# Kernel tuning notes

Measured on AMD Instinct MI355X. Metric: run time of the kernel, lower is better.

## Reference

```python
import jax, jax.numpy as jnp
import numpy as np

N, E = 50000, 800000
F_IN, C1, H1 = 128, 16, 4        # conv1: 128 -> 16 per head, 4 heads (concat -> 64)
F_MID = C1 * H1                   # 64
N_CLASSES, H2 = 10, 1             # conv2: 64 -> 10, 1 head, no concat
NEG_SLOPE = 0.2


def setup_inputs() -> dict:
    key = jax.random.key(0)
    ks = jax.random.split(key, 12)
    s1 = 1.0 / np.sqrt(F_IN)
    s2 = 1.0 / np.sqrt(F_MID)
    return {
        "x": jax.random.normal(ks[0], (N, F_IN), dtype=jnp.float32),
        "edge_index": jax.random.randint(ks[1], (2, E), 0, N, dtype=jnp.int64),
        # conv1 params (GATv2: separate lin_l / lin_r, per-head attention vector, bias)
        "W1l": jax.random.normal(ks[2], (F_IN, H1 * C1), dtype=jnp.float32) * s1,
        "W1r": jax.random.normal(ks[3], (F_IN, H1 * C1), dtype=jnp.float32) * s1,
        "att1": jax.random.normal(ks[4], (H1, C1), dtype=jnp.float32) * s1,
        "b1": jnp.zeros((H1 * C1,), dtype=jnp.float32),
        # conv2 params
        "W2l": jax.random.normal(ks[5], (F_MID, H2 * N_CLASSES), dtype=jnp.float32) * s2,
        "W2r": jax.random.normal(ks[6], (F_MID, H2 * N_CLASSES), dtype=jnp.float32) * s2,
        "att2": jax.random.normal(ks[7], (H2, N_CLASSES), dtype=jnp.float32) * s2,
        "b2": jnp.zeros((N_CLASSES,), dtype=jnp.float32),
    }


def gatv2_conv(x, Wl, Wr, att, b, src, dst, concat):
    """GATv2Conv (add_self_loops=False, eval mode). src -> dst message passing."""
    H, C = att.shape
    n = x.shape[0]
    xl = (x @ Wl).reshape(n, H, C)   # source-side transform (also the value)
    xr = (x @ Wr).reshape(n, H, C)   # target-side transform
    # per-edge GATv2 score: att . LeakyReLU(xl[src] + xr[dst])
    e = jax.nn.leaky_relu(xl[src] + xr[dst], NEG_SLOPE)          # [E, H, C]
    logits = jnp.einsum("ehc,hc->eh", e, att)                    # [E, H]
    # segment softmax over incoming edges of each dst node
    m = jax.ops.segment_max(logits, dst, num_segments=n)         # [N, H]
    ex = jnp.exp(logits - m[dst])
    denom = jax.ops.segment_sum(ex, dst, num_segments=n)         # [N, H]
    alpha = ex / denom[dst]                                      # [E, H]
    out = jax.ops.segment_sum(alpha[:, :, None] * xl[src], dst, num_segments=n)  # [N, H, C]
    out = out.reshape(n, H * C) if concat else out.mean(axis=1)
    return out + b


def reference(x, edge_index, W1l, W1r, att1, b1, W2l, W2r, att2, b2):
    src, dst = edge_index[0], edge_index[1]
    h = jax.nn.elu(gatv2_conv(x, W1l, W1r, att1, b1, src, dst, concat=True))
    return gatv2_conv(h, W2l, W2r, att2, b2, src, dst, concat=False)
```

## Files before the change

### kernel.cpp

```cpp
#include <hip/hip_runtime.h>
#include <math.h>

#define NN 50000
#define NE 800000
#define FIN 128
#define NC 10
#define NEG 0.2f
#define LOG2E 1.4426950408889634f

#define NB 196
#define CHUNK 4096
#define P1B ((NE + CHUNK - 1) / CHUNK)
#define CAP 5120
#define GMT ((NN + 63) / 64)
#define LBW 200
#define WPAD 136

typedef unsigned int uint;
typedef _Float16 h2 __attribute__((ext_vector_type(2)));
typedef _Float16 h8 __attribute__((ext_vector_type(8)));
typedef float f32x4 __attribute__((ext_vector_type(4)));
typedef __fp16 hb2 __attribute__((ext_vector_type(2)));
union U2H { uint u; h2 h; };
union U4H8 { uint4 u; h8 h; };

__device__ __forceinline__ uint pkrtz_u(float a, float b) {
    union { hb2 f; uint u; } r;
    r.f = __builtin_amdgcn_cvt_pkrtz(a, b);
    return r.u;
}

__device__ __forceinline__ float dot2f(h2 a, h2 b, float c) {
#if __has_builtin(__builtin_amdgcn_fdot2)
    return __builtin_amdgcn_fdot2(a, b, c, false);
#else
    return fmaf((float)a.x, (float)b.x, fmaf((float)a.y, (float)b.y, c));
#endif
}

__device__ __forceinline__ h2 lrelu2(h2 v) {
    return __builtin_elementwise_max(v, v * (_Float16)0.2f);
}

template<int CTRL>
__device__ __forceinline__ float dpp_add(float x) {
    int y = __builtin_amdgcn_update_dpp(0, __float_as_int(x), CTRL, 0xF, 0xF, true);
    return x + __int_as_float(y);
}
__device__ __forceinline__ float red8(float t) {
    t = dpp_add<0xB1>(t);
    t = dpp_add<0x4E>(t);
    t = dpp_add<0x141>(t);
    return t;
}

__device__ __forceinline__ int excl_scan256(int v, int* sc) {
    const int t = threadIdx.x;
    sc[t] = v;
    __syncthreads();
    for (int o = 1; o < 256; o <<= 1) {
        int u = (t >= o) ? sc[t - o] : 0;
        __syncthreads();
        sc[t] += u;
        __syncthreads();
    }
    return sc[t] - v;
}


__device__ void pass1_body(const int* __restrict__ ei, uint* __restrict__ temp,
                           int* __restrict__ lbmat, char* smraw) {
    uint* pk = (uint*)smraw;
    int* h   = (int*)(smraw + 16384);
    int* h2_ = (int*)(smraw + 17408);
    int* sc  = (int*)(smraw + 18432);
    const int t = threadIdx.x;
    const int B = blockIdx.x;
    const int e0 = B * CHUNK;
    const int cnt = min(CHUNK, NE - e0);

    h[t] = 0; h2_[t] = 0;
    __syncthreads();
    for (int i = t; i < cnt; i += 256) {
        int d = ei[NE + e0 + i];
        atomicAdd(&h[d >> 8], 1);
    }
    __syncthreads();
    const int hv = h[t];
    const int ex = excl_scan256(hv, sc);
    if (t < NB) lbmat[B * LBW + t] = ex;
    if (t == NB - 1) lbmat[B * LBW + NB] = ex + hv;
    h2_[t] = ex;
    __syncthreads();
    for (int i = t; i < cnt; i += 256) {
        int s = ei[e0 + i];
        int d = ei[NE + e0 + i];
        int b = d >> 8;
        int pos = atomicAdd(&h2_[b], 1);
        pk[pos] = ((uint)s << 8) | ((uint)d & 255u);
    }
    __syncthreads();
    for (int i = t; i < cnt; i += 256) temp[B * CHUNK + i] = pk[i];
}

__device__ void gemm1_body(const float* __restrict__ x,
                           const float* __restrict__ W1l,
                           const float* __restrict__ W1r,
                           _Float16* __restrict__ xlh,
                           _Float16* __restrict__ xrh,
                           int n0, char* smraw) {
    _Float16 (*WtL)[WPAD] = (_Float16(*)[WPAD])smraw;
    _Float16 (*WtR)[WPAD] = (_Float16(*)[WPAD])(smraw + 64 * WPAD * 2);
    const int t = threadIdx.x;

    for (int i = t; i < FIN * 64; i += 256) {
        int k = i >> 6, c = i & 63;
        WtL[c][k] = (_Float16)W1l[i];
        WtR[c][k] = (_Float16)W1r[i];
    }
    __syncthreads();

    const int lane = t & 63;
    const int n0w = n0 + (t >> 6) * 16;
    const int arow = n0w + (lane & 15);
    const int kgrp = (lane >> 4) * 8;
    const int col16 = lane & 15;

    f32x4 acc[8] = {};
    for (int kk = 0; kk < FIN; kk += 32) {
        U4H8 a;
        if (arow < NN) {
            const float4* xp = (const float4*)(x + (size_t)arow * FIN + kk + kgrp);
            float4 v0 = xp[0], v1 = xp[1];
            a.u = make_uint4(pkrtz_u(v0.x, v0.y), pkrtz_u(v0.z, v0.w),
                             pkrtz_u(v1.x, v1.y), pkrtz_u(v1.z, v1.w));
        } else {
            a.u = make_uint4(0u, 0u, 0u, 0u);
        }
        const int kof = kk + kgrp;
#pragma unroll
        for (int ct = 0; ct < 4; ++ct) {
            U4H8 b; b.u = *(const uint4*)&WtL[ct * 16 + col16][kof];
            acc[ct] = __builtin_amdgcn_mfma_f32_16x16x32_f16(a.h, b.h, acc[ct], 0, 0, 0);
        }
#pragma unroll
        for (int ct = 0; ct < 4; ++ct) {
            U4H8 b; b.u = *(const uint4*)&WtR[ct * 16 + col16][kof];
            acc[4 + ct] = __builtin_amdgcn_mfma_f32_16x16x32_f16(a.h, b.h, acc[4 + ct], 0, 0, 0);
        }
    }
    const int crow0 = n0w + (lane >> 4) * 4;
#pragma unroll
    for (int ct = 0; ct < 8; ++ct) {
        _Float16* __restrict__ op = (ct < 4) ? xlh : xrh;
        const int col = (ct & 3) * 16 + col16;
#pragma unroll
        for (int r = 0; r < 4; ++r) {
            int node = crow0 + r;
            if (node < NN) op[(size_t)node * 64 + col] = (_Float16)acc[ct][r];
        }
    }
}

__global__ __launch_bounds__(256) void k_fusedA(const float* __restrict__ x,
                                                const int* __restrict__ ei,
                                                const float* __restrict__ W1l,
                                                const float* __restrict__ W1r,
                                                _Float16* __restrict__ xlh,
                                                _Float16* __restrict__ xrh,
                                                uint* __restrict__ temp,
                                                int* __restrict__ lbmat) {
    __shared__ __align__(16) char smraw[64 * WPAD * 2 * 2];
    if (blockIdx.x < P1B) {
        pass1_body(ei, temp, lbmat, smraw);
    } else {
        int g = blockIdx.x - P1B;
        gemm1_body(x, W1l, W1r, xlh, xrh, g * 64, smraw);
    }
}


__global__ __launch_bounds__(256) void k_pass2(const uint* __restrict__ temp,
                                               const int* __restrict__ lbmat,
                                               int* __restrict__ rowptr,
                                               int* __restrict__ deg,
                                               int* __restrict__ csr_src) {
    __shared__ uint P[CAP];
    __shared__ int nh[256], nbx[256], ncur[256], sc[256];
    const int t = threadIdx.x;
    const int b = blockIdx.x;

    int lbv = 0, len = 0;
    if (t < P1B) {
        lbv = lbmat[t * LBW + b];
        len = lbmat[t * LBW + b + 1] - lbv;
    }
    const int colstart = excl_scan256(len, sc);
    __syncthreads();
    const int cnt = sc[255];
    __syncthreads();
    (void)excl_scan256(lbv, sc);
    __syncthreads();
    const int csrbase = sc[255];
    __syncthreads();
    nh[t] = 0; ncur[t] = 0;
    __syncthreads();
    if (t < P1B) {
        const uint* src = temp + t * CHUNK + lbv;
        for (int i = 0; i < len; ++i) P[colstart + i] = src[i];
    }
    __syncthreads();
    for (int i = t; i < cnt; i += 256) atomicAdd(&nh[P[i] & 255u], 1);
    __syncthreads();
    const int c = nh[t];
    const int nb_ex = excl_scan256(c, sc);
    nbx[t] = nb_ex;
    const int gnode = b * 256 + t;
    if (gnode < NN) { rowptr[gnode] = csrbase + nb_ex; deg[gnode] = c; }
    __syncthreads();
    for (int i = t; i < cnt; i += 256) {
        uint v = P[i];
        int l = (int)(v & 255u);
        int r = atomicAdd(&ncur[l], 1);
        csr_src[csrbase + nbx[l] + r] = (int)(v >> 8);
    }
}


__global__ __launch_bounds__(256) void k_agg1(const uint* __restrict__ xlh2,
                                              const uint* __restrict__ xrh2,
                                              const int* __restrict__ rowptr,
                                              const int* __restrict__ deg,
                                              const int* __restrict__ csr_src,
                                              const float* __restrict__ att1,
                                              const float* __restrict__ b1,
                                              uint* __restrict__ hbh2) {
    const int node = blockIdx.x * 4 + (threadIdx.x >> 6);
    if (node >= NN) return;
    const int lane = threadIdx.x & 63;
    const int fl = lane & 31;
    const int hid = lane >> 5;
    float2 av = *(const float2*)&att1[2 * fl];
    U2H att; att.u = pkrtz_u(av.x * LOG2E, av.y * LOG2E);
    U2H xrf; xrf.u = xrh2[(size_t)node * 32 + fl];
    const int start = rowptr[node];
    const int dg = deg[node];
    const int permbase = (lane & 32) >> 3;

    float denom = 0.f, acc0 = 0.f, acc1 = 0.f;
    for (int base = 0; base < dg; base += 64) {
        int idx = base + lane;
        int srcs = (idx < dg) ? csr_src[start + idx] : 0;
        int rem = dg - base; if (rem > 64) rem = 64;
        int iters = (rem + 1) >> 1;
        int thr = (rem - hid + 1) >> 1;
        for (int jj = 0; jj < iters; jj += 4) {
            int s0 = __builtin_amdgcn_ds_bpermute((jj + 0) * 8 + permbase, srcs);
            int s1 = __builtin_amdgcn_ds_bpermute((jj + 1) * 8 + permbase, srcs);
            int s2 = __builtin_amdgcn_ds_bpermute((jj + 2) * 8 + permbase, srcs);
            int s3 = __builtin_amdgcn_ds_bpermute((jj + 3) * 8 + permbase, srcs);
            U2H v0; v0.u = xlh2[(size_t)s0 * 32 + fl];
            U2H v1; v1.u = xlh2[(size_t)s1 * 32 + fl];
            U2H v2; v2.u = xlh2[(size_t)s2 * 32 + fl];
            U2H v3; v3.u = xlh2[(size_t)s3 * 32 + fl];
            float t0 = red8(dot2f(lrelu2(v0.h + xrf.h), att.h, 0.f));
            float t1 = red8(dot2f(lrelu2(v1.h + xrf.h), att.h, 0.f));
            float t2 = red8(dot2f(lrelu2(v2.h + xrf.h), att.h, 0.f));
            float t3 = red8(dot2f(lrelu2(v3.h + xrf.h), att.h, 0.f));
            float e0 = (jj + 0 < thr) ? exp2f(t0) : 0.f;
            float e1 = (jj + 1 < thr) ? exp2f(t1) : 0.f;
            float e2 = (jj + 2 < thr) ? exp2f(t2) : 0.f;
            float e3 = (jj + 3 < thr) ? exp2f(t3) : 0.f;
            denom += (e0 + e1) + (e2 + e3);
            acc0 = fmaf(e0, (float)v0.h.x, acc0);
            acc0 = fmaf(e1, (float)v1.h.x, acc0);
            acc0 = fmaf(e2, (float)v2.h.x, acc0);
            acc0 = fmaf(e3, (float)v3.h.x, acc0);
            acc1 = fmaf(e0, (float)v0.h.y, acc1);
            acc1 = fmaf(e1, (float)v1.h.y, acc1);
            acc1 = fmaf(e2, (float)v2.h.y, acc1);
            acc1 = fmaf(e3, (float)v3.h.y, acc1);
        }
    }
    denom += __shfl_xor(denom, 32);
    acc0  += __shfl_xor(acc0, 32);
    acc1  += __shfl_xor(acc1, 32);
    if (lane < 32) {
        float r = (dg > 0) ? (1.0f / denom) : 0.f;
        float2 bv = *(const float2*)&b1[2 * fl];
        float o0 = fmaf(acc0, r, bv.x);
        float o1 = fmaf(acc1, r, bv.y);
        o0 = o0 > 0.f ? o0 : expm1f(o0);
        o1 = o1 > 0.f ? o1 : expm1f(o1);
        hbh2[(size_t)node * 32 + fl] = pkrtz_u(o0, o1);
    }
}


__global__ __launch_bounds__(256) void k_gemm2(const uint* __restrict__ hbh2,
                                               const float* __restrict__ W2l,
                                               const float* __restrict__ W2r,
                                               uint* __restrict__ xl2h,
                                               uint* __restrict__ xr2h) {
    int n = blockIdx.x * 256 + threadIdx.x;
    if (n >= NN) return;
    float al[NC] = {}, ar[NC] = {};
    const uint4* hr4 = (const uint4*)(hbh2 + (size_t)n * 32);
#pragma unroll
    for (int q = 0; q < 8; ++q) {
        uint4 qq = hr4[q];
        uint uu[4] = {qq.x, qq.y, qq.z, qq.w};
#pragma unroll
        for (int j = 0; j < 4; ++j) {
            U2H hh; hh.u = uu[j];
            float f0 = (float)hh.h.x, f1 = (float)hh.h.y;
            int k = q * 8 + j * 2;
            const float* wl0 = W2l + k * NC;
            const float* wr0 = W2r + k * NC;
#pragma unroll
            for (int c = 0; c < NC; ++c) {
                al[c] = fmaf(f0, wl0[c], fmaf(f1, wl0[NC + c], al[c]));
                ar[c] = fmaf(f0, wr0[c], fmaf(f1, wr0[NC + c], ar[c]));
            }
        }
    }
    uint p0 = pkrtz_u(al[0], al[1]);
    uint p1 = pkrtz_u(al[2], al[3]);
    uint p2 = pkrtz_u(al[4], al[5]);
    uint p3 = pkrtz_u(al[6], al[7]);
    uint p4 = pkrtz_u(al[8], al[9]);
    *(uint4*)&xl2h[(size_t)n * 8]     = make_uint4(p0, p1, p2, p3);
    *(uint4*)&xl2h[(size_t)n * 8 + 4] = make_uint4(p4, 0u, 0u, 0u);
    p0 = pkrtz_u(ar[0], ar[1]);
    p1 = pkrtz_u(ar[2], ar[3]);
    p2 = pkrtz_u(ar[4], ar[5]);
    p3 = pkrtz_u(ar[6], ar[7]);
    p4 = pkrtz_u(ar[8], ar[9]);
    *(uint4*)&xr2h[(size_t)n * 8]     = make_uint4(p0, p1, p2, p3);
    *(uint4*)&xr2h[(size_t)n * 8 + 4] = make_uint4(p4, 0u, 0u, 0u);
}


__global__ __launch_bounds__(256) void k_agg2(const uint* __restrict__ xl2h,
                                              const uint* __restrict__ xr2h,
                                              const int* __restrict__ rowptr,
                                              const int* __restrict__ deg,
                                              const int* __restrict__ csr_src,
                                              const float* __restrict__ att2,
                                              const float* __restrict__ b2,
                                              float* __restrict__ out) {
    const int node = blockIdx.x * 4 + (threadIdx.x >> 6);
    if (node >= NN) return;
    const int lane = threadIdx.x & 63;
    const int fp = lane & 7;
    const int eg = lane >> 3;
    U2H att;
    if (fp < 5) {
        float2 av = *(const float2*)&att2[2 * fp];
        att.u = pkrtz_u(av.x * LOG2E, av.y * LOG2E);
    } else {
        att.u = 0;
    }
    U2H xrf; xrf.u = xr2h[(size_t)node * 8 + fp];
    const int start = rowptr[node];
    const int dg = deg[node];
    const int permbase = eg * 4;

    float denom = 0.f, acc0 = 0.f, acc1 = 0.f;
    for (int base = 0; base < dg; base += 64) {
        int idx = base + lane;
        int srcs = (idx < dg) ? csr_src[start + idx] : 0;
        int rem = dg - base; if (rem > 64) rem = 64;
        int iters = (rem + 7) >> 3;
        int thr = (rem - eg + 7) >> 3;
        for (int jj = 0; jj < iters; jj += 4) {
            int s[4]; U2H v[4];
#pragma unroll
            for (int k = 0; k < 4; ++k)
                s[k] = __builtin_amdgcn_ds_bpermute((jj + k) * 32 + permbase, srcs);
#pragma unroll
            for (int k = 0; k < 4; ++k)
                v[k].u = xl2h[(size_t)s[k] * 8 + fp];
#pragma unroll
            for (int k = 0; k < 4; ++k) {
                float tl = red8(dot2f(lrelu2(v[k].h + xrf.h), att.h, 0.f));
                float e = (jj + k < thr) ? exp2f(tl) : 0.f;
                denom += e;
                acc0 = fmaf(e, (float)v[k].h.x, acc0);
                acc1 = fmaf(e, (float)v[k].h.y, acc1);
            }
        }
    }
#pragma unroll
    for (int m = 8; m <= 32; m <<= 1) {
        denom += __shfl_xor(denom, m);
        acc0  += __shfl_xor(acc0, m);
        acc1  += __shfl_xor(acc1, m);
    }
    if (lane < 5) {
        float r = (dg > 0) ? (1.0f / denom) : 0.f;
        float2 o;
        o.x = fmaf(acc0, r, b2[2 * fp]);
        o.y = fmaf(acc1, r, b2[2 * fp + 1]);
        *(float2*)&out[(size_t)node * NC + 2 * fp] = o;
    }
}


extern "C" void kernel_launch(void* const* d_in, const int* in_sizes, int n_in,
                              void* d_out, int out_size, void* d_ws, size_t ws_size,
                              hipStream_t stream) {
    const float* x    = (const float*)d_in[0];
    const int*   ei   = (const int*)d_in[1];
    const float* W1l  = (const float*)d_in[2];
    const float* W1r  = (const float*)d_in[3];
    const float* att1 = (const float*)d_in[4];
    const float* b1   = (const float*)d_in[5];
    const float* W2l  = (const float*)d_in[6];
    const float* W2r  = (const float*)d_in[7];
    const float* att2 = (const float*)d_in[8];
    const float* b2   = (const float*)d_in[9];
    float* out = (float*)d_out;

    char* w = (char*)d_ws;
    size_t off = 0;
    auto alloc = [&](size_t bytes) -> void* {
        void* p = w + off;
        off = (off + bytes + 255) & ~(size_t)255;
        return p;
    };
    uint* xlh2   = (uint*)alloc((size_t)NN * 32 * 4);
    uint* xrh2   = (uint*)alloc((size_t)NN * 32 * 4);
    uint* hbh2   = (uint*)alloc((size_t)NN * 32 * 4);
    uint* xl2h   = (uint*)alloc((size_t)NN * 8 * 4);
    uint* xr2h   = (uint*)alloc((size_t)NN * 8 * 4);
    uint* temp   = (uint*)alloc((size_t)P1B * CHUNK * 4);
    int*  lbmat  = (int*)alloc((size_t)P1B * LBW * 4);
    int*  rowptr = (int*)alloc((size_t)NN * 4);
    int*  deg    = (int*)alloc((size_t)NN * 4);
    int*  csr_src = (int*)alloc((size_t)(NE + 64) * 4);

    k_fusedA<<<P1B + GMT, 256, 0, stream>>>(x, ei, W1l, W1r,
                                            (_Float16*)xlh2, (_Float16*)xrh2,
                                            temp, lbmat);
    k_pass2<<<NB, 256, 0, stream>>>(temp, lbmat, rowptr, deg, csr_src);
    k_agg1<<<(NN + 3) / 4, 256, 0, stream>>>(xlh2, xrh2, rowptr, deg, csr_src, att1, b1, hbh2);
    k_gemm2<<<(NN + 255) / 256, 256, 0, stream>>>(hbh2, W2l, W2r, xl2h, xr2h);
    k_agg2<<<(NN + 3) / 4, 256, 0, stream>>>(xl2h, xr2h, rowptr, deg, csr_src, att2, b2, out);
}
```

Baseline: 97.06 us.

## Fuse layer-2 linear transform into layer-1 aggregation kernel

Removes the separate k_gemm2 kernel and the hbh2 intermediate buffer. Each wave now stages its node's ELU output row in shared memory, then 20 lanes compute the 10 left and 10 right layer-2 projections and write xl2h/xr2h directly. This saves one kernel launch and a write-then-read round trip of the hidden features through global memory. In exchange it adds a block-wide barrier and a serial 32-step dot product on a third of the wave's lanes. The early return for out-of-range nodes was dropped, so the last block may read or write past NN unless guarded elsewhere.

```diff
diff --git a/kernel.cpp b/kernel.cpp
--- a/kernel.cpp
+++ b/kernel.cpp
@@ -234,9 +234,13 @@
                                               const int* __restrict__ csr_src,
                                               const float* __restrict__ att1,
                                               const float* __restrict__ b1,
-                                              uint* __restrict__ hbh2) {
-    const int node = blockIdx.x * 4 + (threadIdx.x >> 6);
-    if (node >= NN) return;
+                                              const float* __restrict__ W2l,
+                                              const float* __restrict__ W2r,
+                                              uint* __restrict__ xl2h,
+                                              uint* __restrict__ xr2h) {
+    __shared__ uint hrow[4][32];
+    const int wid = threadIdx.x >> 6;
+    const int node = blockIdx.x * 4 + wid;
     const int lane = threadIdx.x & 63;
     const int fl = lane & 31;
     const int hid = lane >> 5;
@@ -292,52 +296,29 @@
         float o1 = fmaf(acc1, r, bv.y);
         o0 = o0 > 0.f ? o0 : expm1f(o0);
         o1 = o1 > 0.f ? o1 : expm1f(o1);
-        hbh2[(size_t)node * 32 + fl] = pkrtz_u(o0, o1);
-    }
-}
-
-
-__global__ __launch_bounds__(256) void k_gemm2(const uint* __restrict__ hbh2,
-                                               const float* __restrict__ W2l,
-                                               const float* __restrict__ W2r,
-                                               uint* __restrict__ xl2h,
-                                               uint* __restrict__ xr2h) {
-    int n = blockIdx.x * 256 + threadIdx.x;
-    if (n >= NN) return;
-    float al[NC] = {}, ar[NC] = {};
-    const uint4* hr4 = (const uint4*)(hbh2 + (size_t)n * 32);
-#pragma unroll
-    for (int q = 0; q < 8; ++q) {
-        uint4 qq = hr4[q];
-        uint uu[4] = {qq.x, qq.y, qq.z, qq.w};
-#pragma unroll
-        for (int j = 0; j < 4; ++j) {
-            U2H hh; hh.u = uu[j];
-            float f0 = (float)hh.h.x, f1 = (float)hh.h.y;
-            int k = q * 8 + j * 2;
-            const float* wl0 = W2l + k * NC;
-            const float* wr0 = W2r + k * NC;
-#pragma unroll
-            for (int c = 0; c < NC; ++c) {
-                al[c] = fmaf(f0, wl0[c], fmaf(f1, wl0[NC + c], al[c]));
-                ar[c] = fmaf(f0, wr0[c], fmaf(f1, wr0[NC + c], ar[c]));
-            }
-        }
-    }
-    uint p0 = pkrtz_u(al[0], al[1]);
-    uint p1 = pkrtz_u(al[2], al[3]);
-    uint p2 = pkrtz_u(al[4], al[5]);
-    uint p3 = pkrtz_u(al[6], al[7]);
-    uint p4 = pkrtz_u(al[8], al[9]);
-    *(uint4*)&xl2h[(size_t)n * 8]     = make_uint4(p0, p1, p2, p3);
-    *(uint4*)&xl2h[(size_t)n * 8 + 4] = make_uint4(p4, 0u, 0u, 0u);
-    p0 = pkrtz_u(ar[0], ar[1]);
-    p1 = pkrtz_u(ar[2], ar[3]);
-    p2 = pkrtz_u(ar[4], ar[5]);
-    p3 = pkrtz_u(ar[6], ar[7]);
-    p4 = pkrtz_u(ar[8], ar[9]);
-    *(uint4*)&xr2h[(size_t)n * 8]     = make_uint4(p0, p1, p2, p3);
-    *(uint4*)&xr2h[(size_t)n * 8 + 4] = make_uint4(p4, 0u, 0u, 0u);
+        hrow[wid][fl] = pkrtz_u(o0, o1);
+    }
+    __syncthreads();
+    if (lane < 20) {
+        const int side = lane / 10;
+        const int c = lane - side * 10;
+        const float* __restrict__ W2 = side ? W2r : W2l;
+        float acc = 0.f;
+#pragma unroll 8
+        for (int kp = 0; kp < 32; ++kp) {
+            U2H hp; hp.u = hrow[wid][kp];
+            acc = fmaf((float)hp.h.x, W2[(2 * kp) * NC + c],
+                  fmaf((float)hp.h.y, W2[(2 * kp + 1) * NC + c], acc));
+        }
+        float accn = __shfl_down(acc, 1);
+        uint* __restrict__ outp = side ? xr2h : xl2h;
+        if ((c & 1) == 0) outp[(size_t)node * 8 + (c >> 1)] = pkrtz_u(acc, accn);
+        if (c == 0) {
+            outp[(size_t)node * 8 + 5] = 0u;
+            outp[(size_t)node * 8 + 6] = 0u;
+            outp[(size_t)node * 8 + 7] = 0u;
+        }
+    }
 }
 
 
@@ -431,7 +412,6 @@
     };
     uint* xlh2   = (uint*)alloc((size_t)NN * 32 * 4);
     uint* xrh2   = (uint*)alloc((size_t)NN * 32 * 4);
-    uint* hbh2   = (uint*)alloc((size_t)NN * 32 * 4);
     uint* xl2h   = (uint*)alloc((size_t)NN * 8 * 4);
     uint* xr2h   = (uint*)alloc((size_t)NN * 8 * 4);
     uint* temp   = (uint*)alloc((size_t)P1B * CHUNK * 4);
@@ -444,7 +424,7 @@
                                             (_Float16*)xlh2, (_Float16*)xrh2,
                                             temp, lbmat);
     k_pass2<<<NB, 256, 0, stream>>>(temp, lbmat, rowptr, deg, csr_src);
-    k_agg1<<<(NN + 3) / 4, 256, 0, stream>>>(xlh2, xrh2, rowptr, deg, csr_src, att1, b1, hbh2);
-    k_gemm2<<<(NN + 255) / 256, 256, 0, stream>>>(hbh2, W2l, W2r, xl2h, xr2h);
+    k_agg1<<<(NN + 3) / 4, 256, 0, stream>>>(xlh2, xrh2, rowptr, deg, csr_src,
+                                             att1, b1, W2l, W2r, xl2h, xr2h);
     k_agg2<<<(NN + 3) / 4, 256, 0, stream>>>(xl2h, xr2h, rowptr, deg, csr_src, att2, b2, out);
 }
```

New measurement: 112.8 us. +16.2%, slower.
